# Kernel optimization log

Measured on AMD Instinct MI355X. Metric: run time of the kernel, lower is better.

Reference implementation:

```python
import jax, jax.numpy as jnp
import numpy as np

NUM_HEADS = 8
REGION_SIZE = 16
TOPK = 8


def setup_inputs() -> dict:
    key = jax.random.key(0)
    ks = jax.random.split(key, 3)
    B, T, C = 4, 2048, 512
    x = jax.random.normal(ks[0], (B, T, C), dtype=jnp.float32)
    # nn.Linear weights stored as (in, out) so y = x @ W + b
    Wqkv = jax.random.normal(ks[1], (C, 3 * C), dtype=jnp.float32) * 0.02
    bqkv = jnp.zeros((3 * C,), dtype=jnp.float32)
    Wout = jax.random.normal(ks[2], (C, C), dtype=jnp.float32) * 0.02
    bout = jnp.zeros((C,), dtype=jnp.float32)
    return {"x": x, "Wqkv": Wqkv, "bqkv": bqkv, "Wout": Wout, "bout": bout}


def reference(x, Wqkv, bqkv, Wout, bout):
    B, T, C = x.shape
    H, R, K = NUM_HEADS, REGION_SIZE, TOPK
    Dh = C // H
    Nr = T // R  # T chosen divisible by R, so no padding branch
    scale = 1.0 / (Dh ** 0.5)

    qkv = x @ Wqkv + bqkv                                  # (B,T,3C)
    qkv = qkv.reshape(B, T, 3, H, Dh).transpose(2, 0, 3, 1, 4)  # (3,B,H,T,Dh)
    q = qkv[0].reshape(B, H, Nr, R, Dh)
    k = qkv[1].reshape(B, H, Nr, R, Dh)
    v = qkv[2].reshape(B, H, Nr, R, Dh)

    # region-average scores and top-k region selection
    q_avg = q.mean(axis=3)                                 # (B,H,Nr,Dh)
    k_avg = k.mean(axis=3)
    region_score = jnp.einsum('bhqd,bhkd->bhqk', q_avg, k_avg) * scale
    _, topk_idx = jax.lax.top_k(region_score, K)           # (B,H,Nr,K)

    # gather selected K/V region blocks (no dense expand)
    bi = jnp.arange(B)[:, None, None, None]
    hi = jnp.arange(H)[None, :, None, None]
    k_sel = k[bi, hi, topk_idx]                            # (B,H,Nr,K,R,Dh)
    v_sel = v[bi, hi, topk_idx]                            # (B,H,Nr,K,R,Dh)

    # block-sparse attention: each query attends to its K selected regions
    logits = jnp.einsum('bhnrd,bhnksd->bhnrks', q, k_sel) * scale
    logits = logits.reshape(B, H, Nr, R, K * R)
    attn = jax.nn.softmax(logits, axis=-1)
    out = jnp.einsum('bhnrk,bhnkd->bhnrd', attn, v_sel.reshape(B, H, Nr, K * R, Dh))

    out = out.reshape(B, H, T, Dh).transpose(0, 2, 1, 3).reshape(B, T, C)
    return out @ Wout + bout
```

## Files before the change

### kernel.cpp

```cpp
#include <hip/hip_runtime.h>
#include <hip/hip_bf16.h>
#include <math.h>

typedef __bf16 bf16x8 __attribute__((ext_vector_type(8)));
typedef float f32x4 __attribute__((ext_vector_type(4)));

namespace {
constexpr int B  = 4;
constexpr int T  = 2048;
constexpr int C  = 512;
constexpr int H  = 8;
constexpr int Dh = 64;
constexpr int R  = 16;
constexpr int Nr = 128;
constexpr int K  = 8;
constexpr int BT = B * T;
constexpr int QKV_N = 3 * C;
constexpr int KD = 512;
constexpr float SCALE = 0.125f;
}

static __device__ __forceinline__ unsigned short f2bf(float f) {
  unsigned int u = __float_as_uint(f);
  u += 0x7fffu + ((u >> 16) & 1u);
  return (unsigned short)(u >> 16);
}

static __device__ __forceinline__ unsigned cvt_pk_bf16(float lo, float hi) {
  unsigned r;
  asm("v_cvt_pk_bf16_f32 %0, %1, %2" : "=v"(r) : "v"(lo), "v"(hi));
  return r;
}

static __device__ __forceinline__ void gload16(const unsigned short* g, unsigned short* l) {
  __builtin_amdgcn_global_load_lds(
      (const __attribute__((address_space(1))) unsigned int*)g,
      (__attribute__((address_space(3))) unsigned int*)l, 16, 0, 0);
}

__global__ __launch_bounds__(256) void convert_x_kernel(
    const float4* __restrict__ x, ushort4* __restrict__ xbf) {
  const int i = blockIdx.x * 256 + threadIdx.x;
  const float4 v = x[i];
  ushort4 o;
  o.x = f2bf(v.x); o.y = f2bf(v.y); o.z = f2bf(v.z); o.w = f2bf(v.w);
  xbf[i] = o;
}

__global__ __launch_bounds__(256) void transpose_convert_kernel(
    const float* __restrict__ W, unsigned short* __restrict__ Wt, int Kd, int Nd) {
  __shared__ float tile[32][33];
  const int n0 = blockIdx.x * 32, k0 = blockIdx.y * 32;
  const int tx = threadIdx.x & 31, ty = threadIdx.x >> 5;
#pragma unroll
  for (int i = 0; i < 32; i += 8)
    tile[ty + i][tx] = W[(size_t)(k0 + ty + i) * Nd + (n0 + tx)];
  __syncthreads();
#pragma unroll
  for (int i = 0; i < 32; i += 8)
    Wt[(size_t)(n0 + ty + i) * Kd + (k0 + tx)] = f2bf(tile[tx][ty + i]);
}

__device__ __forceinline__ void mfma_mainloop(
    const unsigned short* __restrict__ A, const unsigned short* __restrict__ Bt,
    int bm, int bn, unsigned short* As, unsigned short* Bs, f32x4 (&acc)[4][4]) {
  const int tid = threadIdx.x;
  const int wave = tid >> 6, lane = tid & 63;
  const int wr = wave >> 1, wc = wave & 1;
  const unsigned short* ga = A  + (size_t)(bm + wave * 16 + (lane >> 2)) * KD + (lane & 3) * 8;
  const unsigned short* gb = Bt + (size_t)(bn + wave * 16 + (lane >> 2)) * KD + (lane & 3) * 8;
  unsigned short* lA = As + wave * 512;
  unsigned short* lB = Bs + wave * 512;
  const int fr = lane & 15, kg = lane >> 4;
  const unsigned short* rA = As + (wr * 64 + fr) * 32 + kg * 8;
  const unsigned short* rB = Bs + (wc * 64 + fr) * 32 + kg * 8;
  for (int k0 = 0; k0 < KD; k0 += 32) {
    gload16(ga + k0,                    lA);
    gload16(ga + (size_t)64 * KD + k0,  lA + 2048);
    gload16(gb + k0,                    lB);
    gload16(gb + (size_t)64 * KD + k0,  lB + 2048);
    __syncthreads();
    bf16x8 a[4], b[4];
#pragma unroll
    for (int m = 0; m < 4; ++m) a[m] = *(const bf16x8*)(rA + m * 512);
#pragma unroll
    for (int n = 0; n < 4; ++n) b[n] = *(const bf16x8*)(rB + n * 512);
#pragma unroll
    for (int m = 0; m < 4; ++m)
#pragma unroll
      for (int n = 0; n < 4; ++n)
        acc[m][n] = __builtin_amdgcn_mfma_f32_16x16x32_bf16(a[m], b[n], acc[m][n], 0, 0, 0);
    __syncthreads();
  }
}

__global__ __launch_bounds__(256) void qkv_gemm_mfma_kernel(
    const unsigned short* __restrict__ xbf, const unsigned short* __restrict__ Wt,
    const float* __restrict__ bias,
    unsigned short* __restrict__ qbf, unsigned short* __restrict__ kbf,
    unsigned short* __restrict__ vt) {
  __shared__ unsigned short As[128 * 32];
  __shared__ unsigned short Bs[128 * 32];
  f32x4 acc[4][4] = {};
  const int bm = blockIdx.y * 128, bn = blockIdx.x * 128;
  mfma_mainloop(xbf, Wt, bm, bn, As, Bs, acc);
  const int lane = threadIdx.x & 63, wave = threadIdx.x >> 6;
  const int wr = wave >> 1, wc = wave & 1;
#pragma unroll
  for (int n = 0; n < 4; ++n) {
    const int col = bn + wc * 64 + n * 16 + (lane & 15);
    const int s = col >> 9, h = (col >> 6) & 7, d = col & 63;
    const float bv = bias[col];
#pragma unroll
    for (int m = 0; m < 4; ++m) {
      const int row = bm + wr * 64 + m * 16 + (lane >> 4) * 4;
      const int b = row >> 11, t = row & (T - 1);
      const int bh = b * H + h;
      if (s == 2) {
        ushort4 pk;
        pk.x = f2bf(acc[m][n][0] + bv); pk.y = f2bf(acc[m][n][1] + bv);
        pk.z = f2bf(acc[m][n][2] + bv); pk.w = f2bf(acc[m][n][3] + bv);
        *(ushort4*)&vt[((size_t)bh * Dh + d) * T + t] = pk;
      } else {
        unsigned short* dst = ((s == 0) ? qbf : kbf) + ((size_t)bh * T + t) * Dh + d;
#pragma unroll
        for (int r = 0; r < 4; ++r) dst[(size_t)r * Dh] = f2bf(acc[m][n][r] + bv);
      }
    }
  }
}

__global__ __launch_bounds__(256) void out_gemm_mfma_kernel(
    const unsigned short* __restrict__ Abf, const unsigned short* __restrict__ Wt,
    const float* __restrict__ bias, float* __restrict__ out) {
  __shared__ unsigned short As[128 * 32];
  __shared__ unsigned short Bs[128 * 32];
  f32x4 acc[4][4] = {};
  const int bm = blockIdx.y * 128, bn = blockIdx.x * 128;
  mfma_mainloop(Abf, Wt, bm, bn, As, Bs, acc);
  const int lane = threadIdx.x & 63, wave = threadIdx.x >> 6;
  const int wr = wave >> 1, wc = wave & 1;
#pragma unroll
  for (int n = 0; n < 4; ++n) {
    const int col = bn + wc * 64 + n * 16 + (lane & 15);
    const float bv = bias[col];
#pragma unroll
    for (int m = 0; m < 4; ++m) {
      const int row = bm + wr * 64 + m * 16 + (lane >> 4) * 4;
#pragma unroll
      for (int r = 0; r < 4; ++r)
        out[(size_t)(row + r) * C + col] = acc[m][n][r] + bv;
    }
  }
}

__global__ __launch_bounds__(256) void x_avg_kernel(
    const float* __restrict__ x, float* __restrict__ xavg) {
  const int blk = blockIdx.x;
  const int c = threadIdx.x;
  const float* xp = x + (size_t)blk * R * C;
  float s0 = 0.f, s1 = 0.f;
#pragma unroll
  for (int r = 0; r < R; ++r) { s0 += xp[r * C + c]; s1 += xp[r * C + c + 256]; }
  xavg[(size_t)blk * C + c] = s0 * 0.0625f;
  xavg[(size_t)blk * C + c + 256] = s1 * 0.0625f;
}

__global__ __launch_bounds__(256) void qkavg_gemm_kernel(
    const float* __restrict__ Xa, const float* __restrict__ W,
    const float* __restrict__ bias,
    float* __restrict__ qavg, float* __restrict__ kavg) {
  __shared__ float As[32][68];
  __shared__ float Bs[32][68];
  const int tid = threadIdx.x;
  const int bm = blockIdx.y * 64;
  const int bn = blockIdx.x * 64;
  const int tm4 = (tid >> 4) << 2;
  const int tn4 = (tid & 15) << 2;
  const int arow = tid >> 3;
  const int acol = (tid & 7) << 2;
  const int brow = tid >> 4;
  const int bcol = (tid & 15) << 2;
  float acc[4][4] = {};
  for (int k0 = 0; k0 < KD; k0 += 32) {
#pragma unroll
    for (int p = 0; p < 2; ++p) {
      const float4 a = *(const float4*)&Xa[(size_t)(bm + arow + 32 * p) * KD + (k0 + acol)];
      As[acol + 0][arow + 32 * p] = a.x;
      As[acol + 1][arow + 32 * p] = a.y;
      As[acol + 2][arow + 32 * p] = a.z;
      As[acol + 3][arow + 32 * p] = a.w;
    }
#pragma unroll
    for (int p = 0; p < 2; ++p) {
      *(float4*)&Bs[brow + 16 * p][bcol] =
          *(const float4*)&W[(size_t)(k0 + brow + 16 * p) * QKV_N + (bn + bcol)];
    }
    __syncthreads();
#pragma unroll
    for (int kk = 0; kk < 32; ++kk) {
      const float4 av = *(const float4*)&As[kk][tm4];
      const float4 bv = *(const float4*)&Bs[kk][tn4];
      const float a[4] = {av.x, av.y, av.z, av.w};
      const float bb[4] = {bv.x, bv.y, bv.z, bv.w};
#pragma unroll
      for (int i = 0; i < 4; ++i)
#pragma unroll
        for (int j = 0; j < 4; ++j) acc[i][j] += a[i] * bb[j];
    }
    __syncthreads();
  }
#pragma unroll
  for (int i = 0; i < 4; ++i) {
    const int m = bm + tm4 + i;
    const int b = m >> 7, n = m & (Nr - 1);
#pragma unroll
    for (int j = 0; j < 4; ++j) {
      const int col = bn + tn4 + j;
      const int half = col >> 9, h = (col >> 6) & 7, d = col & 63;
      float* dst = half ? kavg : qavg;
      dst[(((size_t)b * H + h) * Nr + n) * Dh + d] = acc[i][j] + bias[col];
    }
  }
}

__global__ __launch_bounds__(128) void topk_kernel(
    const float* __restrict__ qavg, const float* __restrict__ kavg,
    int* __restrict__ topk) {
  const int blk = blockIdx.x;
  const int bh  = blk >> 7;
  const int m   = threadIdx.x;
  __shared__ float qrow[Dh];
  __shared__ float sc[Nr];
  __shared__ float rv[Nr];
  __shared__ int   ri[Nr];
  __shared__ int   sel[K];
  if (m < Dh) qrow[m] = qavg[(size_t)blk * Dh + m];
  __syncthreads();
  const float* krow = kavg + ((size_t)bh * Nr + m) * Dh;
  float dot = 0.f;
#pragma unroll
  for (int i = 0; i < Dh; ++i) dot += qrow[i] * krow[i];
  sc[m] = dot;
  bool taken = false;
  __syncthreads();
  for (int j = 0; j < K; ++j) {
    rv[m] = taken ? -INFINITY : sc[m];
    ri[m] = m;
    __syncthreads();
    for (int off = 64; off >= 1; off >>= 1) {
      if (m < off) {
        const float v2 = rv[m + off]; const int i2 = ri[m + off];
        if (v2 > rv[m] || (v2 == rv[m] && i2 < ri[m])) { rv[m] = v2; ri[m] = i2; }
      }
      __syncthreads();
    }
    if (m == 0) sel[j] = ri[0];
    __syncthreads();
    if (m == sel[j]) taken = true;
  }
  if (m < K) topk[blk * K + m] = sel[m];
}

__global__ __launch_bounds__(64) void attn_mfma_kernel(
    const unsigned short* __restrict__ qbf, const unsigned short* __restrict__ kbf,
    const unsigned short* __restrict__ vt, const int* __restrict__ topk,
    unsigned short* __restrict__ aoutbf) {
  const int phys = blockIdx.x;
  const int blk = (phys & 7) * 512 + (phys >> 3);
  const int bh = blk >> 7, n = blk & (Nr - 1);
  const int b = bh >> 3, h = bh & 7;
  const int lane = threadIdx.x;
  const int q = lane & 15, kg = lane >> 4;
  const int kg1 = kg & 1, kgh = kg >> 1;

  const int rv = topk[blk * K + (lane & 7)];
  int ridx[8];
#pragma unroll
  for (int j = 0; j < 8; ++j) ridx[j] = __shfl(rv, j);

  const unsigned short* qp = qbf + ((size_t)bh * T + n * R + q) * Dh + kg * 8;
  const bf16x8 qf0 = *(const bf16x8*)(qp);
  const bf16x8 qf1 = *(const bf16x8*)(qp + 32);

  f32x4 s[8];
#pragma unroll
  for (int j = 0; j < 8; ++j) {
    const unsigned short* kp = kbf + ((size_t)bh * T + ridx[j] * R + q) * Dh + kg * 8;
    const bf16x8 kf0 = *(const bf16x8*)(kp);
    const bf16x8 kf1 = *(const bf16x8*)(kp + 32);
    f32x4 acc = {};
    acc = __builtin_amdgcn_mfma_f32_16x16x32_bf16(kf0, qf0, acc, 0, 0, 0);
    acc = __builtin_amdgcn_mfma_f32_16x16x32_bf16(kf1, qf1, acc, 0, 0, 0);
    s[j] = acc;
  }

  float mx = s[0][0];
#pragma unroll
  for (int j = 0; j < 8; ++j)
#pragma unroll
    for (int r = 0; r < 4; ++r) mx = fmaxf(mx, s[j][r]);
  mx = fmaxf(mx, __shfl_xor(mx, 16));
  mx = fmaxf(mx, __shfl_xor(mx, 32));
  float sum = 0.f;
#pragma unroll
  for (int j = 0; j < 8; ++j)
#pragma unroll
    for (int r = 0; r < 4; ++r) {
      const float e = __expf((s[j][r] - mx) * SCALE);
      s[j][r] = e; sum += e;
    }
  sum += __shfl_xor(sum, 16);
  sum += __shfl_xor(sum, 32);

  unsigned pk0[8], pk1[8];
#pragma unroll
  for (int j = 0; j < 8; ++j) {
    pk0[j] = cvt_pk_bf16(s[j][0], s[j][1]);
    pk1[j] = cvt_pk_bf16(s[j][2], s[j][3]);
  }

  const int srcA = kg1 * 32 + q;
  const int srcB = kg1 * 32 + 16 + q;
  f32x4 o[4] = {};
#pragma unroll
  for (int t = 0; t < 4; ++t) {
    const unsigned aa0 = __shfl((int)pk0[2 * t], srcA), aa1 = __shfl((int)pk0[2 * t + 1], srcA);
    const unsigned ab0 = __shfl((int)pk1[2 * t], srcA), ab1 = __shfl((int)pk1[2 * t + 1], srcA);
    const unsigned ba0 = __shfl((int)pk0[2 * t], srcB), ba1 = __shfl((int)pk0[2 * t + 1], srcB);
    const unsigned bb0 = __shfl((int)pk1[2 * t], srcB), bb1 = __shfl((int)pk1[2 * t + 1], srcB);
    union { uint4 u; bf16x8 v; } bu;
    bu.u.x = kgh ? aa1 : aa0;
    bu.u.y = kgh ? ab1 : ab0;
    bu.u.z = kgh ? ba1 : ba0;
    bu.u.w = kgh ? bb1 : bb0;
    const int reg = kgh ? ridx[2 * t + 1] : ridx[2 * t];
    const size_t tok = (size_t)reg * R + kg1 * 8;
#pragma unroll
    for (int dt = 0; dt < 4; ++dt) {
      const bf16x8 af = *(const bf16x8*)(vt + ((size_t)bh * Dh + 16 * dt + q) * T + tok);
      o[dt] = __builtin_amdgcn_mfma_f32_16x16x32_bf16(af, bu.v, o[dt], 0, 0, 0);
    }
  }

  const float inv = 1.0f / sum;
  unsigned short* dst = aoutbf + ((size_t)b * T + n * R + q) * C + h * Dh;
#pragma unroll
  for (int dt = 0; dt < 4; ++dt) {
    const unsigned plo = cvt_pk_bf16(o[dt][0] * inv, o[dt][1] * inv);
    const unsigned phi = cvt_pk_bf16(o[dt][2] * inv, o[dt][3] * inv);
    uint2 st; st.x = plo; st.y = phi;
    *(uint2*)(dst + 16 * dt + kg * 4) = st;
  }
}

extern "C" void kernel_launch(void* const* d_in, const int* in_sizes, int n_in,
                              void* d_out, int out_size, void* d_ws, size_t ws_size,
                              hipStream_t stream) {
  const float* x    = (const float*)d_in[0];
  const float* Wqkv = (const float*)d_in[1];
  const float* bqkv = (const float*)d_in[2];
  const float* Wout = (const float*)d_in[3];
  const float* bout = (const float*)d_in[4];
  float* out = (float*)d_out;

  float* ws = (float*)d_ws;
  const size_t bhtd = (size_t)B * H * T * Dh;
  const size_t navg = (size_t)B * H * Nr * Dh;
  float* qavg = ws;
  float* kavg = qavg + navg;
  float* xavg = kavg + navg;
  unsigned short* qbf    = (unsigned short*)(xavg + navg);
  unsigned short* kbf    = qbf + bhtd;
  unsigned short* vt     = kbf + bhtd;
  unsigned short* xbf    = vt + bhtd;
  unsigned short* wqkvt  = xbf + bhtd;
  unsigned short* woutt  = wqkvt + (size_t)QKV_N * KD;
  unsigned short* aoutbf = woutt + (size_t)C * KD;
  int* topk = (int*)(aoutbf + bhtd);

  convert_x_kernel<<<4096, 256, 0, stream>>>((const float4*)x, (ushort4*)xbf);
  transpose_convert_kernel<<<dim3(QKV_N / 32, KD / 32), 256, 0, stream>>>(Wqkv, wqkvt, KD, QKV_N);
  transpose_convert_kernel<<<dim3(C / 32, KD / 32), 256, 0, stream>>>(Wout, woutt, KD, C);
  x_avg_kernel<<<B * Nr, 256, 0, stream>>>(x, xavg);
  qkavg_gemm_kernel<<<dim3(1024 / 64, (B * Nr) / 64), 256, 0, stream>>>(xavg, Wqkv, bqkv, qavg, kavg);
  topk_kernel<<<B * H * Nr, 128, 0, stream>>>(qavg, kavg, topk);
  qkv_gemm_mfma_kernel<<<dim3(QKV_N / 128, BT / 128), 256, 0, stream>>>(xbf, wqkvt, bqkv, qbf, kbf, vt);
  attn_mfma_kernel<<<B * H * Nr, 64, 0, stream>>>(qbf, kbf, vt, topk, aoutbf);
  out_gemm_mfma_kernel<<<dim3(C / 128, BT / 128), 256, 0, stream>>>(aoutbf, woutt, bout, out);
}
```

Baseline: 137.3 us.

## Warp-shuffle topk, vectorized QKV stores, XCD-aware block remap, retune qkavg GEMM

Rewrites the top-k kernel as a single wavefront that computes scores with float4 loads and selects via 64-bit packed key shuffle reductions, removing shared-memory reductions and many barriers. The QKV GEMM epilogue packs bf16 pairs and transposes through lane shuffles so Q/K rows are written as 8-byte stores instead of scattered 2-byte stores. Both MFMA GEMMs use a 1D grid remapped so consecutive tiles land on the same XCD for L2 reuse. The qkavg GEMM doubles its thread count with smaller per-thread tiles. The tie-breaking in top-k is kept at lower index first via the packed inverted index.

After: 132.4 us. -3.6%, faster.

```diff
diff --git a/kernel.cpp b/kernel.cpp
--- a/kernel.cpp
+++ b/kernel.cpp
@@ -36,6 +36,11 @@
   __builtin_amdgcn_global_load_lds(
       (const __attribute__((address_space(1))) unsigned int*)g,
       (__attribute__((address_space(3))) unsigned int*)l, 16, 0, 0);
+}
+
+static __device__ __forceinline__ unsigned fkey(float f) {
+  unsigned u = __float_as_uint(f);
+  return (u & 0x80000000u) ? ~u : (u ^ 0x80000000u);
 }
 
 __global__ __launch_bounds__(256) void convert_x_kernel(
@@ -102,29 +107,55 @@
   __shared__ unsigned short As[128 * 32];
   __shared__ unsigned short Bs[128 * 32];
   f32x4 acc[4][4] = {};
-  const int bm = blockIdx.y * 128, bn = blockIdx.x * 128;
+  const int id = (blockIdx.x & 7) * 96 + (blockIdx.x >> 3);
+  const int bn = (id % 12) * 128, bm = (id / 12) * 128;
   mfma_mainloop(xbf, Wt, bm, bn, As, Bs, acc);
   const int lane = threadIdx.x & 63, wave = threadIdx.x >> 6;
   const int wr = wave >> 1, wc = wave & 1;
-#pragma unroll
-  for (int n = 0; n < 4; ++n) {
-    const int col = bn + wc * 64 + n * 16 + (lane & 15);
-    const int s = col >> 9, h = (col >> 6) & 7, d = col & 63;
-    const float bv = bias[col];
-#pragma unroll
-    for (int m = 0; m < 4; ++m) {
-      const int row = bm + wr * 64 + m * 16 + (lane >> 4) * 4;
-      const int b = row >> 11, t = row & (T - 1);
-      const int bh = b * H + h;
-      if (s == 2) {
+  const int scol = bn + wc * 64;
+  const int s = scol >> 9, h = (scol >> 6) & 7;
+  const int b = bm >> 11, t0b = (bm & (T - 1)) + wr * 64;
+  const int bh = b * H + h;
+  if (s == 2) {
+#pragma unroll
+    for (int n = 0; n < 4; ++n) {
+      const int d = (n * 16 + (lane & 15));
+      const float bv = bias[scol + n * 16 + (lane & 15)];
+#pragma unroll
+      for (int m = 0; m < 4; ++m) {
+        const int t = t0b + m * 16 + (lane >> 4) * 4;
         ushort4 pk;
         pk.x = f2bf(acc[m][n][0] + bv); pk.y = f2bf(acc[m][n][1] + bv);
         pk.z = f2bf(acc[m][n][2] + bv); pk.w = f2bf(acc[m][n][3] + bv);
         *(ushort4*)&vt[((size_t)bh * Dh + d) * T + t] = pk;
-      } else {
-        unsigned short* dst = ((s == 0) ? qbf : kbf) + ((size_t)bh * T + t) * Dh + d;
-#pragma unroll
-        for (int r = 0; r < 4; ++r) dst[(size_t)r * Dh] = f2bf(acc[m][n][r] + bv);
+      }
+    }
+  } else {
+    unsigned short* dstbase = ((s == 0) ? qbf : kbf) + (size_t)bh * T * Dh;
+    const int g = lane >> 4, i = lane & 3, a = (lane >> 2) & 3;
+#pragma unroll
+    for (int n = 0; n < 4; ++n) {
+      const float bv = bias[scol + n * 16 + (lane & 15)];
+#pragma unroll
+      for (int m = 0; m < 4; ++m) {
+        const float v0 = acc[m][n][0] + bv, v1 = acc[m][n][1] + bv;
+        const float v2 = acc[m][n][2] + bv, v3 = acc[m][n][3] + bv;
+        const unsigned p01 = cvt_pk_bf16(v0, v1);
+        const unsigned p23 = cvt_pk_bf16(v2, v3);
+        const unsigned u01 = (unsigned)__shfl_xor((int)p01, 1);
+        const unsigned u23 = (unsigned)__shfl_xor((int)p23, 1);
+        const unsigned A  = (lane & 1) ? ((u01 >> 16) | (p01 & 0xFFFF0000u))
+                                       : ((p01 & 0xFFFFu) | (u01 << 16));
+        const unsigned Bb = (lane & 1) ? ((u23 >> 16) | (p23 & 0xFFFF0000u))
+                                       : ((p23 & 0xFFFFu) | (u23 << 16));
+        const unsigned w  = (unsigned)__shfl_xor((int)A, 2);
+        const unsigned xw = (unsigned)__shfl_xor((int)Bb, 2);
+        uint2 res;
+        res.x = (lane & 2) ? xw : A;
+        res.y = (lane & 2) ? Bb : w;
+        const int t = t0b + m * 16 + 4 * g + i;
+        const int d = n * 16 + 4 * a;
+        *(uint2*)&dstbase[(size_t)t * Dh + d] = res;
       }
     }
   }
@@ -136,7 +167,8 @@
   __shared__ unsigned short As[128 * 32];
   __shared__ unsigned short Bs[128 * 32];
   f32x4 acc[4][4] = {};
-  const int bm = blockIdx.y * 128, bn = blockIdx.x * 128;
+  const int id = (blockIdx.x & 7) * 32 + (blockIdx.x >> 3);
+  const int bn = (id & 3) * 128, bm = (id >> 2) * 128;
   mfma_mainloop(Abf, Wt, bm, bn, As, Bs, acc);
   const int lane = threadIdx.x & 63, wave = threadIdx.x >> 6;
   const int wr = wave >> 1, wc = wave & 1;
@@ -166,7 +198,7 @@
   xavg[(size_t)blk * C + c + 256] = s1 * 0.0625f;
 }
 
-__global__ __launch_bounds__(256) void qkavg_gemm_kernel(
+__global__ __launch_bounds__(512) void qkavg_gemm_kernel(
     const float* __restrict__ Xa, const float* __restrict__ W,
     const float* __restrict__ bias,
     float* __restrict__ qavg, float* __restrict__ kavg) {
@@ -175,48 +207,44 @@
   const int tid = threadIdx.x;
   const int bm = blockIdx.y * 64;
   const int bn = blockIdx.x * 64;
-  const int tm4 = (tid >> 4) << 2;
-  const int tn4 = (tid & 15) << 2;
+  const int tm = (tid >> 5) << 2;
+  const int tn = (tid & 31) << 1;
   const int arow = tid >> 3;
   const int acol = (tid & 7) << 2;
   const int brow = tid >> 4;
   const int bcol = (tid & 15) << 2;
-  float acc[4][4] = {};
+  float acc[4][2] = {};
   for (int k0 = 0; k0 < KD; k0 += 32) {
-#pragma unroll
-    for (int p = 0; p < 2; ++p) {
-      const float4 a = *(const float4*)&Xa[(size_t)(bm + arow + 32 * p) * KD + (k0 + acol)];
-      As[acol + 0][arow + 32 * p] = a.x;
-      As[acol + 1][arow + 32 * p] = a.y;
-      As[acol + 2][arow + 32 * p] = a.z;
-      As[acol + 3][arow + 32 * p] = a.w;
-    }
-#pragma unroll
-    for (int p = 0; p < 2; ++p) {
-      *(float4*)&Bs[brow + 16 * p][bcol] =
-          *(const float4*)&W[(size_t)(k0 + brow + 16 * p) * QKV_N + (bn + bcol)];
+    {
+      const float4 a = *(const float4*)&Xa[(size_t)(bm + arow) * KD + (k0 + acol)];
+      As[acol + 0][arow] = a.x;
+      As[acol + 1][arow] = a.y;
+      As[acol + 2][arow] = a.z;
+      As[acol + 3][arow] = a.w;
+      *(float4*)&Bs[brow][bcol] =
+          *(const float4*)&W[(size_t)(k0 + brow) * QKV_N + (bn + bcol)];
     }
     __syncthreads();
 #pragma unroll
     for (int kk = 0; kk < 32; ++kk) {
-      const float4 av = *(const float4*)&As[kk][tm4];
-      const float4 bv = *(const float4*)&Bs[kk][tn4];
-      const float a[4] = {av.x, av.y, av.z, av.w};
-      const float bb[4] = {bv.x, bv.y, bv.z, bv.w};
-#pragma unroll
-      for (int i = 0; i < 4; ++i)
-#pragma unroll
-        for (int j = 0; j < 4; ++j) acc[i][j] += a[i] * bb[j];
+      const float4 av = *(const float4*)&As[kk][tm];
+      const float2 bv = *(const float2*)&Bs[kk][tn];
+      const float aa[4] = {av.x, av.y, av.z, av.w};
+#pragma unroll
+      for (int i = 0; i < 4; ++i) {
+        acc[i][0] += aa[i] * bv.x;
+        acc[i][1] += aa[i] * bv.y;
+      }
     }
     __syncthreads();
   }
 #pragma unroll
   for (int i = 0; i < 4; ++i) {
-    const int m = bm + tm4 + i;
+    const int m = bm + tm + i;
     const int b = m >> 7, n = m & (Nr - 1);
 #pragma unroll
-    for (int j = 0; j < 4; ++j) {
-      const int col = bn + tn4 + j;
+    for (int j = 0; j < 2; ++j) {
+      const int col = bn + tn + j;
       const int half = col >> 9, h = (col >> 6) & 7, d = col & 63;
       float* dst = half ? kavg : qavg;
       dst[(((size_t)b * H + h) * Nr + n) * Dh + d] = acc[i][j] + bias[col];
@@ -224,42 +252,45 @@
   }
 }
 
-__global__ __launch_bounds__(128) void topk_kernel(
+__global__ __launch_bounds__(64) void topk_kernel(
     const float* __restrict__ qavg, const float* __restrict__ kavg,
     int* __restrict__ topk) {
   const int blk = blockIdx.x;
   const int bh  = blk >> 7;
-  const int m   = threadIdx.x;
-  __shared__ float qrow[Dh];
-  __shared__ float sc[Nr];
-  __shared__ float rv[Nr];
-  __shared__ int   ri[Nr];
-  __shared__ int   sel[K];
-  if (m < Dh) qrow[m] = qavg[(size_t)blk * Dh + m];
-  __syncthreads();
-  const float* krow = kavg + ((size_t)bh * Nr + m) * Dh;
-  float dot = 0.f;
-#pragma unroll
-  for (int i = 0; i < Dh; ++i) dot += qrow[i] * krow[i];
-  sc[m] = dot;
-  bool taken = false;
-  __syncthreads();
+  const int lane = threadIdx.x;
+  const float qv = qavg[(size_t)blk * Dh + lane];
+  const float4* k0p = (const float4*)(kavg + ((size_t)bh * Nr + lane) * Dh);
+  const float4* k1p = (const float4*)(kavg + ((size_t)bh * Nr + lane + 64) * Dh);
+  float d0 = 0.f, d1 = 0.f;
+#pragma unroll
+  for (int j = 0; j < 16; ++j) {
+    const float4 a = k0p[j];
+    const float4 bq = k1p[j];
+    const float q0 = __shfl(qv, 4 * j + 0);
+    const float q1 = __shfl(qv, 4 * j + 1);
+    const float q2 = __shfl(qv, 4 * j + 2);
+    const float q3 = __shfl(qv, 4 * j + 3);
+    d0 += q0 * a.x;  d0 += q1 * a.y;  d0 += q2 * a.z;  d0 += q3 * a.w;
+    d1 += q0 * bq.x; d1 += q1 * bq.y; d1 += q2 * bq.z; d1 += q3 * bq.w;
+  }
+  float v0 = d0, v1 = d1;
+#pragma unroll
   for (int j = 0; j < K; ++j) {
-    rv[m] = taken ? -INFINITY : sc[m];
-    ri[m] = m;
-    __syncthreads();
-    for (int off = 64; off >= 1; off >>= 1) {
-      if (m < off) {
-        const float v2 = rv[m + off]; const int i2 = ri[m + off];
-        if (v2 > rv[m] || (v2 == rv[m] && i2 < ri[m])) { rv[m] = v2; ri[m] = i2; }
-      }
-      __syncthreads();
-    }
-    if (m == 0) sel[j] = ri[0];
-    __syncthreads();
-    if (m == sel[j]) taken = true;
-  }
-  if (m < K) topk[blk * K + m] = sel[m];
+    const unsigned long long c0 =
+        ((unsigned long long)fkey(v0) << 32) | (unsigned)(127 - lane);
+    const unsigned long long c1 =
+        ((unsigned long long)fkey(v1) << 32) | (unsigned)(63 - lane);
+    unsigned long long c = (c0 > c1) ? c0 : c1;
+#pragma unroll
+    for (int off = 1; off < 64; off <<= 1) {
+      const unsigned long long o = __shfl_xor(c, off);
+      c = (o > c) ? o : c;
+    }
+    const int idx = 127 - (int)(c & 0xffffffffu);
+    if (lane == j) topk[blk * K + j] = idx;
+    if (idx == lane) v0 = -INFINITY;
+    if (idx == lane + 64) v1 = -INFINITY;
+  }
 }
 
 __global__ __launch_bounds__(64) void attn_mfma_kernel(
@@ -383,9 +414,9 @@
   transpose_convert_kernel<<<dim3(QKV_N / 32, KD / 32), 256, 0, stream>>>(Wqkv, wqkvt, KD, QKV_N);
   transpose_convert_kernel<<<dim3(C / 32, KD / 32), 256, 0, stream>>>(Wout, woutt, KD, C);
   x_avg_kernel<<<B * Nr, 256, 0, stream>>>(x, xavg);
-  qkavg_gemm_kernel<<<dim3(1024 / 64, (B * Nr) / 64), 256, 0, stream>>>(xavg, Wqkv, bqkv, qavg, kavg);
-  topk_kernel<<<B * H * Nr, 128, 0, stream>>>(qavg, kavg, topk);
-  qkv_gemm_mfma_kernel<<<dim3(QKV_N / 128, BT / 128), 256, 0, stream>>>(xbf, wqkvt, bqkv, qbf, kbf, vt);
+  qkavg_gemm_kernel<<<dim3(1024 / 64, (B * Nr) / 64), 512, 0, stream>>>(xavg, Wqkv, bqkv, qavg, kavg);
+  topk_kernel<<<B * H * Nr, 64, 0, stream>>>(qavg, kavg, topk);
+  qkv_gemm_mfma_kernel<<<QKV_N / 128 * (BT / 128), 256, 0, stream>>>(xbf, wqkvt, bqkv, qbf, kbf, vt);
   attn_mfma_kernel<<<B * H * Nr, 64, 0, stream>>>(qbf, kbf, vt, topk, aoutbf);
-  out_gemm_mfma_kernel<<<dim3(C / 128, BT / 128), 256, 0, stream>>>(aoutbf, woutt, bout, out);
-}
+  out_gemm_mfma_kernel<<<C / 128 * (BT / 128), 256, 0, stream>>>(aoutbf, woutt, bout, out);
+}
```
